# Performance work log

Hardware: AMD Instinct MI355X
Metric: run time of the kernel (lower is better)

The kernel has to match this reference:

```python
import jax, jax.numpy as jnp
import numpy as np

B, N, D, H = 2, 2048, 1024, 16
DH = D // H  # 64 per-head dim before LRPE
EPS = 1e-5


def setup_inputs() -> dict:
    key = jax.random.key(0)
    ks = jax.random.split(key, 8)
    x = jax.random.normal(ks[0], (B, N, D), dtype=jnp.float32)
    context = jax.random.normal(ks[1], (B, N, D), dtype=jnp.float32)
    Wqkvu = jax.random.normal(ks[2], (4 * D, D), dtype=jnp.float32) * 0.02
    bqkvu = jax.random.normal(ks[3], (4 * D,), dtype=jnp.float32) * 0.02
    Wout = jax.random.normal(ks[4], (D, D), dtype=jnp.float32) * 0.02
    bout = jax.random.normal(ks[5], (D,), dtype=jnp.float32) * 0.02
    # Lrpe theta: 10000**(-2/d * arange(d)) reshaped to (H, 1, DH)
    theta = (10000.0 ** (-2.0 / D * jnp.arange(D, dtype=jnp.float32))).reshape(H, 1, DH)
    ln_w = jnp.ones((D,), dtype=jnp.float32)
    ln_b = jnp.zeros((D,), dtype=jnp.float32)
    return {"x": x, "context": context, "Wqkvu": Wqkvu, "bqkvu": bqkvu,
            "Wout": Wout, "bout": bout, "theta": theta, "ln_w": ln_w, "ln_b": ln_b}


def _lrpe(t, theta, n):
    # t: [b,h,n,d]; theta: [h,1,d]; index: [1,n,1]
    idx = jnp.arange(n, dtype=t.dtype).reshape(1, n, 1)
    th = theta * idx  # [h,n,d]
    return jnp.concatenate([t * jnp.cos(th), t * jnp.sin(th)], axis=-1)  # [b,h,n,2d]


def reference(x, context, Wqkvu, bqkvu, Wout, bout, theta, ln_w, ln_b):
    b, n, d = x.shape
    qkvu = x @ Wqkvu.T + bqkvu  # [b,n,4d]
    q, k, v, u = jnp.split(qkvu, 4, axis=-1)
    tohead = lambda t: t.reshape(b, n, H, DH).transpose(0, 2, 1, 3)  # b h n d
    q, k, v = tohead(q), tohead(k), tohead(v)
    q = jax.nn.silu(q)
    k = jax.nn.silu(k)
    q = _lrpe(q, theta, n)  # [b,h,n,2*DH]
    k = _lrpe(k, theta, n)
    # left form: materialize qk then contract with v
    qk = jnp.einsum('bhmd,bhnd->bhmn', q, k)
    out = jnp.einsum('bhmn,bhne->bhme', qk, v)  # [b,h,n,DH]
    out = out.transpose(0, 2, 1, 3).reshape(b, n, d)
    # LayerNorm
    mu = jnp.mean(out, axis=-1, keepdims=True)
    var = jnp.var(out, axis=-1, keepdims=True)
    out = (out - mu) * jax.lax.rsqrt(var + EPS) * ln_w + ln_b
    out = u * out
    return out @ Wout.T + bout
```

## Files before the change

kernel.cpp:

```cpp
#include <hip/hip_runtime.h>
#include <math.h>

#define B_ 2
#define N_ 2048
#define D_ 1024
#define H_ 16
#define DH_ 64
#define ROWS (B_*N_)
#define FOURD (4*D_)
#define EPS_ 1e-5f

typedef short bf16x8 __attribute__((ext_vector_type(8)));
typedef unsigned short u16x8 __attribute__((ext_vector_type(8)));
typedef float f32x4  __attribute__((ext_vector_type(4)));

__device__ __forceinline__ unsigned short f2bf(float f) {
    unsigned int x = __float_as_uint(f);
    unsigned int r = (x + 0x7fffu + ((x >> 16) & 1u)) >> 16;
    return (unsigned short)r;
}
__device__ __forceinline__ float bf2f(unsigned short u) {
    return __uint_as_float((unsigned int)u << 16);
}

__global__ __launch_bounds__(256)
void cast_f32_bf16(const float* __restrict__ in, unsigned short* __restrict__ out, int n4)
{
    int i = blockIdx.x * 256 + threadIdx.x;
    if (i >= n4) return;
    float4 v = ((const float4*)in)[i];
    ushort4 o;
    o.x = f2bf(v.x); o.y = f2bf(v.y); o.z = f2bf(v.z); o.w = f2bf(v.w);
    ((ushort4*)out)[i] = o;
}

__global__ __launch_bounds__(256)
void gemm_bt_128(const unsigned short* __restrict__ A,
                 const unsigned short* __restrict__ Bw,
                 const float* __restrict__ bias, unsigned short* __restrict__ C,
                 int M, int N, int K, int siluLim)
{
    __shared__ unsigned short As[128 * 32];
    __shared__ unsigned short Bs[128 * 32];

    const int tid  = threadIdx.x;
    const int row0 = blockIdx.y * 128;
    const int col0 = blockIdx.x * 128;
    const int wave = tid >> 6;
    const int lane = tid & 63;
    const int wr   = (wave >> 1) * 64;
    const int wc   = (wave & 1) * 64;
    const int l15  = lane & 15;
    const int quad = lane >> 4;

    f32x4 acc[4][4] = {};

    const int srow = tid >> 2;
    const int skk  = (tid & 3) * 8;
    const unsigned short* ag = A  + (size_t)(row0 + srow) * K + skk;
    const unsigned short* bg = Bw + (size_t)(col0 + srow) * K + skk;

    typedef const __attribute__((address_space(1))) unsigned int* gp_t;
    typedef __attribute__((address_space(3))) unsigned int* lp_t;
    lp_t asd = (lp_t)(void*)&As[tid * 8];
    lp_t bsd = (lp_t)(void*)&Bs[tid * 8];

    for (int k0 = 0; k0 < K; k0 += 32) {
        __builtin_amdgcn_global_load_lds((gp_t)(const void*)(ag + k0),                asd,        16, 0, 0);
        __builtin_amdgcn_global_load_lds((gp_t)(const void*)(ag + (size_t)64*K + k0), asd + 1024, 16, 0, 0);
        __builtin_amdgcn_global_load_lds((gp_t)(const void*)(bg + k0),                bsd,        16, 0, 0);
        __builtin_amdgcn_global_load_lds((gp_t)(const void*)(bg + (size_t)64*K + k0), bsd + 1024, 16, 0, 0);
        __syncthreads();

        bf16x8 af[4], bfr[4];
#pragma unroll
        for (int i = 0; i < 4; ++i)
            af[i] = *(const bf16x8*)&As[(wr + i * 16 + l15) * 32 + quad * 8];
#pragma unroll
        for (int j = 0; j < 4; ++j)
            bfr[j] = *(const bf16x8*)&Bs[(wc + j * 16 + l15) * 32 + quad * 8];
#pragma unroll
        for (int i = 0; i < 4; ++i)
#pragma unroll
            for (int j = 0; j < 4; ++j)
                acc[i][j] = __builtin_amdgcn_mfma_f32_16x16x32_bf16(af[i], bfr[j], acc[i][j], 0, 0, 0);
        __syncthreads();
    }

#pragma unroll
    for (int i = 0; i < 4; ++i) {
        const int r0 = row0 + wr + i * 16 + quad * 4;
#pragma unroll
        for (int j = 0; j < 4; ++j) {
            const int c = col0 + wc + j * 16 + l15;
            const float bb = bias[c];
#pragma unroll
            for (int r = 0; r < 4; ++r) {
                float v = acc[i][j][r] + bb;
                if (c < siluLim) v = v / (1.f + expf(-v));
                C[(size_t)(r0 + r) * N + c] = f2bf(v);
            }
        }
    }
}

__global__ __launch_bounds__(256)
void gemm_bt_64(const unsigned short* __restrict__ A,
                const unsigned short* __restrict__ Bw,
                const float* __restrict__ bias, float* __restrict__ C,
                int M, int N, int K)
{
    __shared__ unsigned short As[128 * 32];
    __shared__ unsigned short Bs[64 * 32];

    const int tid  = threadIdx.x;
    const int row0 = blockIdx.y * 128;
    const int col0 = blockIdx.x * 64;
    const int wave = tid >> 6;
    const int lane = tid & 63;
    const int wr   = wave * 32;
    const int l15  = lane & 15;
    const int quad = lane >> 4;

    f32x4 acc[2][4] = {};

    const int srow = tid >> 2;
    const int skk  = (tid & 3) * 8;
    const unsigned short* ag = A  + (size_t)(row0 + srow) * K + skk;
    const unsigned short* bg = Bw + (size_t)(col0 + srow) * K + skk;

    typedef const __attribute__((address_space(1))) unsigned int* gp_t;
    typedef __attribute__((address_space(3))) unsigned int* lp_t;
    lp_t asd = (lp_t)(void*)&As[tid * 8];
    lp_t bsd = (lp_t)(void*)&Bs[tid * 8];

    for (int k0 = 0; k0 < K; k0 += 32) {
        __builtin_amdgcn_global_load_lds((gp_t)(const void*)(ag + k0),                asd,        16, 0, 0);
        __builtin_amdgcn_global_load_lds((gp_t)(const void*)(ag + (size_t)64*K + k0), asd + 1024, 16, 0, 0);
        __builtin_amdgcn_global_load_lds((gp_t)(const void*)(bg + k0),                bsd,        16, 0, 0);
        __syncthreads();

        bf16x8 af[2], bfr[4];
#pragma unroll
        for (int i = 0; i < 2; ++i)
            af[i] = *(const bf16x8*)&As[(wr + i * 16 + l15) * 32 + quad * 8];
#pragma unroll
        for (int j = 0; j < 4; ++j)
            bfr[j] = *(const bf16x8*)&Bs[(j * 16 + l15) * 32 + quad * 8];
#pragma unroll
        for (int i = 0; i < 2; ++i)
#pragma unroll
            for (int j = 0; j < 4; ++j)
                acc[i][j] = __builtin_amdgcn_mfma_f32_16x16x32_bf16(af[i], bfr[j], acc[i][j], 0, 0, 0);
        __syncthreads();
    }

#pragma unroll
    for (int i = 0; i < 2; ++i) {
        const int r0 = row0 + wr + i * 16 + quad * 4;
#pragma unroll
        for (int j = 0; j < 4; ++j) {
            const int c = col0 + j * 16 + l15;
            const float bb = bias[c];
#pragma unroll
            for (int r = 0; r < 4; ++r)
                C[(size_t)(r0 + r) * N + c] = acc[i][j][r] + bb;
        }
    }
}

__global__ __launch_bounds__(256)
void kv_mfma(const unsigned short* __restrict__ qkvu, const float* __restrict__ theta,
             float* __restrict__ part)
{
    __shared__ unsigned short kl_s[128][136];
    __shared__ unsigned short v_s [64][136];

    const int bid   = blockIdx.x;
    const int chunk = bid & 15;
    const int bh    = bid >> 4;
    const int h     = bh & 15;
    const int b     = bh >> 4;
    const int tid   = threadIdx.x;
    const int lane  = tid & 63;
    const int wave  = tid >> 6;
    const int l15   = lane & 15;
    const int quad  = lane >> 4;
    const int n0    = chunk * 128;

    for (int i = tid; i < 1024; i += 256) {
        const int nn  = i >> 3;
        const int dh0 = (i & 7) * 8;
        const int n   = n0 + nn;
        const unsigned short* qrow = qkvu + (size_t)(b * N_ + n) * FOURD;
        u16x8 k8 = *(const u16x8*)(qrow + D_     + h * DH_ + dh0);
        u16x8 v8 = *(const u16x8*)(qrow + 2 * D_ + h * DH_ + dh0);
#pragma unroll
        for (int j = 0; j < 8; ++j) {
            const int dh = dh0 + j;
            const float kf = bf2f(k8[j]);
            float s, c; sincosf(theta[h * DH_ + dh] * (float)n, &s, &c);
            kl_s[dh][nn]      = f2bf(kf * c);
            kl_s[64 + dh][nn] = f2bf(kf * s);
            v_s[dh][nn]       = v8[j];
        }
    }
    __syncthreads();

    f32x4 acc[2][4] = {};
#pragma unroll
    for (int ks = 0; ks < 4; ++ks) {
        bf16x8 a0 = *(const bf16x8*)&kl_s[wave * 32 +      l15][ks * 32 + quad * 8];
        bf16x8 a1 = *(const bf16x8*)&kl_s[wave * 32 + 16 + l15][ks * 32 + quad * 8];
#pragma unroll
        for (int j = 0; j < 4; ++j) {
            bf16x8 bfr = *(const bf16x8*)&v_s[j * 16 + l15][ks * 32 + quad * 8];
            acc[0][j] = __builtin_amdgcn_mfma_f32_16x16x32_bf16(a0, bfr, acc[0][j], 0, 0, 0);
            acc[1][j] = __builtin_amdgcn_mfma_f32_16x16x32_bf16(a1, bfr, acc[1][j], 0, 0, 0);
        }
    }

    float* pp = part + ((size_t)bh * 16 + chunk) * 8192;
#pragma unroll
    for (int i = 0; i < 2; ++i) {
        const int d0 = wave * 32 + i * 16 + quad * 4;
#pragma unroll
        for (int j = 0; j < 4; ++j) {
            const int e = j * 16 + l15;
#pragma unroll
            for (int r = 0; r < 4; ++r)
                pp[(d0 + r) * 64 + e] = acc[i][j][r];
        }
    }
}

__global__ __launch_bounds__(256)
void kv_reduce(const float* __restrict__ part, float* __restrict__ kv)
{
    const int i  = blockIdx.x * 256 + threadIdx.x;
    const int bh = i >> 13;
    const float* pp = part + ((size_t)bh * 16) * 8192 + (i & 8191);
    float s = 0.f;
#pragma unroll
    for (int c = 0; c < 16; ++c) s += pp[c * 8192];
    kv[i] = s;
}

__global__ __launch_bounds__(256)
void attn_ln_kernel(const unsigned short* __restrict__ qkvu, const float* __restrict__ kvb,
                    const float* __restrict__ theta, const float* __restrict__ ln_w,
                    const float* __restrict__ ln_b, unsigned short* __restrict__ g)
{
    __shared__ float qc_s[8][1024];
    __shared__ float qs_s[8][1024];
    __shared__ float red[4][16];
    __shared__ float mured[8], rsred[8];

    const int row0 = blockIdx.x * 8;
    const int b    = row0 >> 11;
    const int tid  = threadIdx.x;
    const int lane = tid & 63;
    const int wave = tid >> 6;

    for (int i = tid; i < 2048; i += 256) {
        const int r  = i >> 8;
        const int c0 = (i & 255) * 4;
        const int n  = (row0 + r) & (N_ - 1);
        ushort4 qv = *(const ushort4*)&qkvu[(size_t)(row0 + r) * FOURD + c0];
        float4 tv = *(const float4*)&theta[c0];
        float q[4] = {bf2f(qv.x), bf2f(qv.y), bf2f(qv.z), bf2f(qv.w)};
        float t[4] = {tv.x, tv.y, tv.z, tv.w};
        float4 cv, sv;
        float* cp = (float*)&cv; float* sp = (float*)&sv;
#pragma unroll
        for (int j = 0; j < 4; ++j) {
            float s, c; sincosf(t[j] * (float)n, &s, &c);
            cp[j] = q[j] * c; sp[j] = q[j] * s;
        }
        *(float4*)&qc_s[r][c0] = cv;
        *(float4*)&qs_s[r][c0] = sv;
    }
    __syncthreads();

    const int c0 = tid * 4;
    const int h  = c0 >> 6;
    const int e0 = c0 & 63;
    const float* kvp = kvb + (size_t)(b * H_ + h) * 8192;

    float o[8][4] = {};
    for (int d = 0; d < 64; ++d) {
        float4 kc = *(const float4*)&kvp[d * 64 + e0];
        float4 ks = *(const float4*)&kvp[(64 + d) * 64 + e0];
#pragma unroll
        for (int r = 0; r < 8; ++r) {
            const float qc = qc_s[r][h * 64 + d];
            const float qs = qs_s[r][h * 64 + d];
            o[r][0] = fmaf(qc, kc.x, fmaf(qs, ks.x, o[r][0]));
            o[r][1] = fmaf(qc, kc.y, fmaf(qs, ks.y, o[r][1]));
            o[r][2] = fmaf(qc, kc.z, fmaf(qs, ks.z, o[r][2]));
            o[r][3] = fmaf(qc, kc.w, fmaf(qs, ks.w, o[r][3]));
        }
    }

    float sum[8], sq[8];
#pragma unroll
    for (int r = 0; r < 8; ++r) {
        sum[r] = o[r][0] + o[r][1] + o[r][2] + o[r][3];
        sq[r]  = o[r][0]*o[r][0] + o[r][1]*o[r][1] + o[r][2]*o[r][2] + o[r][3]*o[r][3];
    }
#pragma unroll
    for (int off = 32; off; off >>= 1)
#pragma unroll
        for (int r = 0; r < 8; ++r) {
            sum[r] += __shfl_down(sum[r], off, 64);
            sq[r]  += __shfl_down(sq[r],  off, 64);
        }
    if (lane == 0)
#pragma unroll
        for (int r = 0; r < 8; ++r) { red[wave][r] = sum[r]; red[wave][8 + r] = sq[r]; }
    __syncthreads();
    if (tid < 8) {
        const float s  = red[0][tid] + red[1][tid] + red[2][tid] + red[3][tid];
        const float q2 = red[0][8+tid] + red[1][8+tid] + red[2][8+tid] + red[3][8+tid];
        const float mu = s * (1.f / (float)D_);
        const float var = q2 * (1.f / (float)D_) - mu * mu;
        mured[tid] = mu;
        rsred[tid] = rsqrtf(var + EPS_);
    }
    __syncthreads();

    float4 wv = *(const float4*)&ln_w[c0];
    float4 bv = *(const float4*)&ln_b[c0];
#pragma unroll
    for (int r = 0; r < 8; ++r) {
        ushort4 uvb = *(const ushort4*)&qkvu[(size_t)(row0 + r) * FOURD + 3 * D_ + c0];
        const float mu = mured[r], rs = rsred[r];
        ushort4 ov;
        ov.x = f2bf(((o[r][0] - mu) * rs * wv.x + bv.x) * bf2f(uvb.x));
        ov.y = f2bf(((o[r][1] - mu) * rs * wv.y + bv.y) * bf2f(uvb.y));
        ov.z = f2bf(((o[r][2] - mu) * rs * wv.z + bv.z) * bf2f(uvb.z));
        ov.w = f2bf(((o[r][3] - mu) * rs * wv.w + bv.w) * bf2f(uvb.w));
        *(ushort4*)&g[(size_t)(row0 + r) * D_ + c0] = ov;
    }
}

extern "C" void kernel_launch(void* const* d_in, const int* in_sizes, int n_in,
                              void* d_out, int out_size, void* d_ws, size_t ws_size,
                              hipStream_t stream)
{
    const float* x     = (const float*)d_in[0];
    const float* Wqkvu = (const float*)d_in[2];
    const float* bqkvu = (const float*)d_in[3];
    const float* Wout  = (const float*)d_in[4];
    const float* bout  = (const float*)d_in[5];
    const float* theta = (const float*)d_in[6];
    const float* ln_w  = (const float*)d_in[7];
    const float* ln_b  = (const float*)d_in[8];
    float* out = (float*)d_out;

    char* ws = (char*)d_ws;
    unsigned short* qkvu  = (unsigned short*)ws; ws += (size_t)ROWS * FOURD * 2;
    float*          kvbuf = (float*)ws;          ws += (size_t)B_ * H_ * 8192 * 4;
    unsigned short* wqb   = (unsigned short*)ws; ws += (size_t)FOURD * D_ * 2;
    unsigned short* wob   = (unsigned short*)ws; ws += (size_t)D_ * D_ * 2;
    unsigned short* xb    = (unsigned short*)ws; ws += (size_t)ROWS * D_ * 2;
    float*          part  = (float*)ws;
    unsigned short* gb    = (unsigned short*)ws;

    dim3 blk(256);
    cast_f32_bf16<<<dim3(ROWS * D_ / 4 / 256), blk, 0, stream>>>(x, xb, ROWS * D_ / 4);
    cast_f32_bf16<<<dim3(FOURD * D_ / 4 / 256), blk, 0, stream>>>(Wqkvu, wqb, FOURD * D_ / 4);
    cast_f32_bf16<<<dim3(D_ * D_ / 4 / 256), blk, 0, stream>>>(Wout, wob, D_ * D_ / 4);

    gemm_bt_128<<<dim3(FOURD / 128, ROWS / 128), blk, 0, stream>>>(
        xb, wqb, bqkvu, qkvu, ROWS, FOURD, D_, 2 * D_);
    kv_mfma<<<dim3(32 * 16), blk, 0, stream>>>(qkvu, theta, part);
    kv_reduce<<<dim3(32 * 8192 / 256), blk, 0, stream>>>(part, kvbuf);
    attn_ln_kernel<<<dim3(ROWS / 8), blk, 0, stream>>>(qkvu, kvbuf, theta, ln_w, ln_b, gb);
    gemm_bt_64<<<dim3(D_ / 64, ROWS / 128), blk, 0, stream>>>(
        gb, wob, bout, out, ROWS, D_, D_);
}
```

Before: 232.6 us.

## Widen GEMM K-tile to 64 with XOR-swizzled LDS, fuse casts, use fast intrinsics

Both GEMMs now stage 64-wide K tiles per iteration instead of 32, halving the number of barrier pairs, and apply an XOR swizzle to LDS column slots to reduce bank conflicts on the fragment reads. The three cast kernels are merged into one launch. The SiLU exp and the LRPE sincos calls switch to fast intrinsics (__expf, __sincosf). The fast sincos loses accuracy for large arguments (theta*n can reach about 2047), which risks numerical error.

```diff
diff --git a/kernel.cpp b/kernel.cpp
--- a/kernel.cpp
+++ b/kernel.cpp
@@ -14,6 +14,9 @@
 typedef unsigned short u16x8 __attribute__((ext_vector_type(8)));
 typedef float f32x4  __attribute__((ext_vector_type(4)));
 
+typedef const __attribute__((address_space(1))) unsigned int* gp_t;
+typedef __attribute__((address_space(3))) unsigned int* lp_t;
+
 __device__ __forceinline__ unsigned short f2bf(float f) {
     unsigned int x = __float_as_uint(f);
     unsigned int r = (x + 0x7fffu + ((x >> 16) & 1u)) >> 16;
@@ -24,14 +27,19 @@
 }
 
 __global__ __launch_bounds__(256)
-void cast_f32_bf16(const float* __restrict__ in, unsigned short* __restrict__ out, int n4)
+void cast_all(const float* __restrict__ x, const float* __restrict__ w1,
+              const float* __restrict__ w2, unsigned short* __restrict__ xb,
+              unsigned short* __restrict__ w1b, unsigned short* __restrict__ w2b)
 {
     int i = blockIdx.x * 256 + threadIdx.x;
-    if (i >= n4) return;
-    float4 v = ((const float4*)in)[i];
+    const float* src; unsigned short* dst; int off;
+    if (i < 1048576)      { src = x;  dst = xb;  off = i; }
+    else if (i < 2097152) { src = w1; dst = w1b; off = i - 1048576; }
+    else                  { src = w2; dst = w2b; off = i - 2097152; }
+    float4 v = ((const float4*)src)[off];
     ushort4 o;
     o.x = f2bf(v.x); o.y = f2bf(v.y); o.z = f2bf(v.z); o.w = f2bf(v.w);
-    ((ushort4*)out)[i] = o;
+    ((ushort4*)dst)[off] = o;
 }
 
 __global__ __launch_bounds__(256)
@@ -40,8 +48,8 @@
                  const float* __restrict__ bias, unsigned short* __restrict__ C,
                  int M, int N, int K, int siluLim)
 {
-    __shared__ unsigned short As[128 * 32];
-    __shared__ unsigned short Bs[128 * 32];
+    __shared__ unsigned short As[128 * 64];
+    __shared__ unsigned short Bs[128 * 64];
 
     const int tid  = threadIdx.x;
     const int row0 = blockIdx.y * 128;
@@ -52,38 +60,41 @@
     const int wc   = (wave & 1) * 64;
     const int l15  = lane & 15;
     const int quad = lane >> 4;
+    const int xr   = l15 & 7;
 
     f32x4 acc[4][4] = {};
 
-    const int srow = tid >> 2;
-    const int skk  = (tid & 3) * 8;
+    const int srow = tid >> 3;
+    const int skk  = ((tid & 7) ^ (srow & 7)) * 8;
     const unsigned short* ag = A  + (size_t)(row0 + srow) * K + skk;
     const unsigned short* bg = Bw + (size_t)(col0 + srow) * K + skk;
-
-    typedef const __attribute__((address_space(1))) unsigned int* gp_t;
-    typedef __attribute__((address_space(3))) unsigned int* lp_t;
     lp_t asd = (lp_t)(void*)&As[tid * 8];
     lp_t bsd = (lp_t)(void*)&Bs[tid * 8];
 
-    for (int k0 = 0; k0 < K; k0 += 32) {
-        __builtin_amdgcn_global_load_lds((gp_t)(const void*)(ag + k0),                asd,        16, 0, 0);
-        __builtin_amdgcn_global_load_lds((gp_t)(const void*)(ag + (size_t)64*K + k0), asd + 1024, 16, 0, 0);
-        __builtin_amdgcn_global_load_lds((gp_t)(const void*)(bg + k0),                bsd,        16, 0, 0);
-        __builtin_amdgcn_global_load_lds((gp_t)(const void*)(bg + (size_t)64*K + k0), bsd + 1024, 16, 0, 0);
+    for (int k0 = 0; k0 < K; k0 += 64) {
+#pragma unroll
+        for (int s = 0; s < 4; ++s) {
+            __builtin_amdgcn_global_load_lds((gp_t)(const void*)(ag + (size_t)(32 * s) * K + k0), asd + s * 1024, 16, 0, 0);
+            __builtin_amdgcn_global_load_lds((gp_t)(const void*)(bg + (size_t)(32 * s) * K + k0), bsd + s * 1024, 16, 0, 0);
+        }
         __syncthreads();
 
-        bf16x8 af[4], bfr[4];
-#pragma unroll
-        for (int i = 0; i < 4; ++i)
-            af[i] = *(const bf16x8*)&As[(wr + i * 16 + l15) * 32 + quad * 8];
-#pragma unroll
-        for (int j = 0; j < 4; ++j)
-            bfr[j] = *(const bf16x8*)&Bs[(wc + j * 16 + l15) * 32 + quad * 8];
-#pragma unroll
-        for (int i = 0; i < 4; ++i)
+#pragma unroll
+        for (int ksub = 0; ksub < 2; ++ksub) {
+            const int slot = ((ksub * 4 + quad) ^ xr) * 8;
+            bf16x8 af[4], bfr[4];
+#pragma unroll
+            for (int i = 0; i < 4; ++i)
+                af[i] = *(const bf16x8*)&As[(wr + i * 16 + l15) * 64 + slot];
 #pragma unroll
             for (int j = 0; j < 4; ++j)
-                acc[i][j] = __builtin_amdgcn_mfma_f32_16x16x32_bf16(af[i], bfr[j], acc[i][j], 0, 0, 0);
+                bfr[j] = *(const bf16x8*)&Bs[(wc + j * 16 + l15) * 64 + slot];
+#pragma unroll
+            for (int i = 0; i < 4; ++i)
+#pragma unroll
+                for (int j = 0; j < 4; ++j)
+                    acc[i][j] = __builtin_amdgcn_mfma_f32_16x16x32_bf16(af[i], bfr[j], acc[i][j], 0, 0, 0);
+        }
         __syncthreads();
     }
 
@@ -97,7 +108,7 @@
 #pragma unroll
             for (int r = 0; r < 4; ++r) {
                 float v = acc[i][j][r] + bb;
-                if (c < siluLim) v = v / (1.f + expf(-v));
+                if (c < siluLim) v = v / (1.f + __expf(-v));
                 C[(size_t)(r0 + r) * N + c] = f2bf(v);
             }
         }
@@ -110,8 +121,8 @@
                 const float* __restrict__ bias, float* __restrict__ C,
                 int M, int N, int K)
 {
-    __shared__ unsigned short As[128 * 32];
-    __shared__ unsigned short Bs[64 * 32];
+    __shared__ unsigned short As[128 * 64];
+    __shared__ unsigned short Bs[64 * 64];
 
     const int tid  = threadIdx.x;
     const int row0 = blockIdx.y * 128;
@@ -121,37 +132,42 @@
     const int wr   = wave * 32;
     const int l15  = lane & 15;
     const int quad = lane >> 4;
+    const int xr   = l15 & 7;
 
     f32x4 acc[2][4] = {};
 
-    const int srow = tid >> 2;
-    const int skk  = (tid & 3) * 8;
+    const int srow = tid >> 3;
+    const int skk  = ((tid & 7) ^ (srow & 7)) * 8;
     const unsigned short* ag = A  + (size_t)(row0 + srow) * K + skk;
     const unsigned short* bg = Bw + (size_t)(col0 + srow) * K + skk;
-
-    typedef const __attribute__((address_space(1))) unsigned int* gp_t;
-    typedef __attribute__((address_space(3))) unsigned int* lp_t;
     lp_t asd = (lp_t)(void*)&As[tid * 8];
     lp_t bsd = (lp_t)(void*)&Bs[tid * 8];
 
-    for (int k0 = 0; k0 < K; k0 += 32) {
-        __builtin_amdgcn_global_load_lds((gp_t)(const void*)(ag + k0),                asd,        16, 0, 0);
-        __builtin_amdgcn_global_load_lds((gp_t)(const void*)(ag + (size_t)64*K + k0), asd + 1024, 16, 0, 0);
-        __builtin_amdgcn_global_load_lds((gp_t)(const void*)(bg + k0),                bsd,        16, 0, 0);
+    for (int k0 = 0; k0 < K; k0 += 64) {
+#pragma unroll
+        for (int s = 0; s < 4; ++s)
+            __builtin_amdgcn_global_load_lds((gp_t)(const void*)(ag + (size_t)(32 * s) * K + k0), asd + s * 1024, 16, 0, 0);
+#pragma unroll
+        for (int s = 0; s < 2; ++s)
+            __builtin_amdgcn_global_load_lds((gp_t)(const void*)(bg + (size_t)(32 * s) * K + k0), bsd + s * 1024, 16, 0, 0);
         __syncthreads();
 
-        bf16x8 af[2], bfr[4];
-#pragma unroll
-        for (int i = 0; i < 2; ++i)
-            af[i] = *(const bf16x8*)&As[(wr + i * 16 + l15) * 32 + quad * 8];
-#pragma unroll
-        for (int j = 0; j < 4; ++j)
-            bfr[j] = *(const bf16x8*)&Bs[(j * 16 + l15) * 32 + quad * 8];
-#pragma unroll
-        for (int i = 0; i < 2; ++i)
+#pragma unroll
+        for (int ksub = 0; ksub < 2; ++ksub) {
+            const int slot = ((ksub * 4 + quad) ^ xr) * 8;
+            bf16x8 af[2], bfr[4];
+#pragma unroll
+            for (int i = 0; i < 2; ++i)
+                af[i] = *(const bf16x8*)&As[(wr + i * 16 + l15) * 64 + slot];
 #pragma unroll
             for (int j = 0; j < 4; ++j)
-                acc[i][j] = __builtin_amdgcn_mfma_f32_16x16x32_bf16(af[i], bfr[j], acc[i][j], 0, 0, 0);
+                bfr[j] = *(const bf16x8*)&Bs[(j * 16 + l15) * 64 + slot];
+#pragma unroll
+            for (int i = 0; i < 2; ++i)
+#pragma unroll
+                for (int j = 0; j < 4; ++j)
+                    acc[i][j] = __builtin_amdgcn_mfma_f32_16x16x32_bf16(af[i], bfr[j], acc[i][j], 0, 0, 0);
+        }
         __syncthreads();
     }
 
@@ -199,7 +215,7 @@
         for (int j = 0; j < 8; ++j) {
             const int dh = dh0 + j;
             const float kf = bf2f(k8[j]);
-            float s, c; sincosf(theta[h * DH_ + dh] * (float)n, &s, &c);
+            float s, c; __sincosf(theta[h * DH_ + dh] * (float)n, &s, &c);
             kl_s[dh][nn]      = f2bf(kf * c);
             kl_s[64 + dh][nn] = f2bf(kf * s);
             v_s[dh][nn]       = v8[j];
@@ -274,7 +290,7 @@
         float* cp = (float*)&cv; float* sp = (float*)&sv;
 #pragma unroll
         for (int j = 0; j < 4; ++j) {
-            float s, c; sincosf(t[j] * (float)n, &s, &c);
+            float s, c; __sincosf(t[j] * (float)n, &s, &c);
             cp[j] = q[j] * c; sp[j] = q[j] * s;
         }
         *(float4*)&qc_s[r][c0] = cv;
@@ -368,9 +384,7 @@
     unsigned short* gb    = (unsigned short*)ws;
 
     dim3 blk(256);
-    cast_f32_bf16<<<dim3(ROWS * D_ / 4 / 256), blk, 0, stream>>>(x, xb, ROWS * D_ / 4);
-    cast_f32_bf16<<<dim3(FOURD * D_ / 4 / 256), blk, 0, stream>>>(Wqkvu, wqb, FOURD * D_ / 4);
-    cast_f32_bf16<<<dim3(D_ * D_ / 4 / 256), blk, 0, stream>>>(Wout, wob, D_ * D_ / 4);
+    cast_all<<<dim3(2359296 / 256), blk, 0, stream>>>(x, Wqkvu, Wout, xb, wqb, wob);
 
     gemm_bt_128<<<dim3(FOURD / 128, ROWS / 128), blk, 0, stream>>>(
         xb, wqb, bqkvu, qkvu, ROWS, FOURD, D_, 2 * D_);
```

Measured after the change: 210.1 us. 1.11x faster.
